# Kernel tuning notes

Hardware: AMD Instinct MI355X
Metric: run time of the kernel (lower is better)

Reference implementation:

```python
import jax, jax.numpy as jnp
import numpy as np

EPS = 1e-7  # tf.keras.backend.epsilon()


def squash(v, axis=-1):
    s = jnp.sum(jnp.square(v), axis=axis, keepdims=True)
    scale = s / (1.0 + s) / jnp.sqrt(s + EPS)
    return scale * v


def setup_inputs() -> dict:
    key = jax.random.key(0)
    k1, k2 = jax.random.split(key)
    B, I, D = 64, 2048, 16   # batch, input_num_capsule, input_dim_capsule
    J, K = 32, 16            # num_capsule, dim_capsule
    inputs = jax.random.normal(k1, (B, I, D), dtype=jnp.float32)
    # glorot_uniform-ish init for W: [in_caps, num_caps, in_dim, dim_caps]
    limit = np.sqrt(6.0 / (D + K)).astype(np.float32)
    W = jax.random.uniform(k2, (I, J, D, K), dtype=jnp.float32, minval=-limit, maxval=limit)
    return {"inputs": inputs, "W": W}


def reference(inputs, W, routings=3):
    # u_hat[b,i,j,:] = inputs[b,i,:] @ W[i,j,:,:]
    u_hat = jnp.einsum('bid,ijdk->bijk', inputs, W)  # [B, I, J, K]
    B, I, J, _ = u_hat.shape
    b = jnp.zeros((B, I, J, 1), dtype=u_hat.dtype)
    outputs = None
    for r in range(routings):
        c = jax.nn.softmax(b, axis=2)                              # [B, I, J, 1]
        outputs = squash(jnp.sum(c * u_hat, axis=1, keepdims=True))  # [B, 1, J, K]
        if r < routings - 1:
            b = b + jnp.sum(u_hat * outputs, axis=-1, keepdims=True)
    return jnp.squeeze(outputs, axis=1)  # [B, J, K]
```

## Files before the change

### kernel.cpp

```cpp
#include <hip/hip_runtime.h>
#include <hip/hip_bf16.h>


#define B_ 64
#define I_ 2048
#define D_ 16
#define J_ 32
#define K_ 16
#define JK 512
#define NBLK 256
#define GI 8

typedef __attribute__((ext_vector_type(8))) short short8;
typedef __attribute__((ext_vector_type(4))) float float4v;

__device__ __forceinline__ unsigned short f2bf(float f) {
    union { float f; unsigned int i; } v;
    v.f = f;
    const unsigned int x = v.i;
    return (unsigned short)((x + 0x7fffu + ((x >> 16) & 1u)) >> 16);
}

template <int MODE>
__global__ __launch_bounds__(512)
void caps_pass(const float* __restrict__ x, const float* __restrict__ W,
               const float* __restrict__ vsum, float* __restrict__ part) {
    __shared__ unsigned short wlds[2][32 * 384];
    __shared__ unsigned short zbuf[8];
    __shared__ float ebuf[2][4][2][16];
    const int tid = threadIdx.x;
    const int lane = tid & 63;
    const int wv = tid >> 6;
    const int bt = wv & 3;
    const int jh = wv >> 2;
    const int quad = lane >> 4;
    const int l15 = lane & 15;
    const int b = bt * 16 + l15;
    const int i0 = blockIdx.x * GI;

    if (tid < 8) zbuf[tid] = 0;

    float4 vv[16];
    if (MODE == 1) {
#pragma unroll
        for (int jj = 0; jj < 16; ++jj)
            vv[jj] = reinterpret_cast<const float4*>(
                vsum + b * JK + (jh * 16 + jj) * 16 + quad * 4)[0];
    }

    float4 acc2[16];
#pragma unroll
    for (int jj = 0; jj < 16; ++jj) {
        acc2[jj].x = 0.f; acc2[jj].y = 0.f;
        acc2[jj].z = 0.f; acc2[jj].w = 0.f;
    }

    const int sk = tid & 15;
    const int sj = tid >> 4;

    for (int t = 0; t < GI; ++t) {
        const int i = i0 + t;
        const int par = t & 1;

        {
            const float* p = W + (size_t)i * (J_ * D_ * K_) + sj * (D_ * K_) + sk;
            float vals[16];
#pragma unroll
            for (int d = 0; d < 16; ++d) vals[d] = p[d * K_];
            unsigned int pk[8];
#pragma unroll
            for (int q = 0; q < 8; ++q)
                pk[q] = ((unsigned int)f2bf(vals[2 * q + 1]) << 16) |
                        f2bf(vals[2 * q]);
            uint4* dst = reinterpret_cast<uint4*>(&wlds[par][sj * 384 + sk * 24]);
            uint4 w0; w0.x = pk[0]; w0.y = pk[1]; w0.z = pk[2]; w0.w = pk[3];
            uint4 w1; w1.x = pk[4]; w1.y = pk[5]; w1.z = pk[6]; w1.w = pk[7];
            dst[0] = w0; dst[1] = w1;
        }

        union { uint4 u; short8 s; } bfrag;
        {
            const float* xp = x + ((size_t)b * I_ + i) * D_ + (quad & 1) * 8;
            const float4 x0 = reinterpret_cast<const float4*>(xp)[0];
            const float4 x1 = reinterpret_cast<const float4*>(xp)[1];
            bfrag.u.x = ((unsigned int)f2bf(x0.y) << 16) | f2bf(x0.x);
            bfrag.u.y = ((unsigned int)f2bf(x0.w) << 16) | f2bf(x0.z);
            bfrag.u.z = ((unsigned int)f2bf(x1.y) << 16) | f2bf(x1.x);
            bfrag.u.w = ((unsigned int)f2bf(x1.w) << 16) | f2bf(x1.z);
            if (quad >= 2) { bfrag.u.x = 0; bfrag.u.y = 0; bfrag.u.z = 0; bfrag.u.w = 0; }
        }
        __syncthreads();

        const unsigned short* aptr =
            (quad >= 2) ? zbuf : (&wlds[par][0] + l15 * 24 + (quad & 1) * 8);
        const int astride = (quad >= 2) ? 0 : 384;

        if (MODE == 0) {
#pragma unroll
            for (int jj = 0; jj < 16; ++jj) {
                const int j = jh * 16 + jj;
                union { uint4 u; short8 s; } af;
                af.u = *reinterpret_cast<const uint4*>(aptr + (size_t)j * astride);
                float4v a = {0.f, 0.f, 0.f, 0.f};
                a = __builtin_amdgcn_mfma_f32_16x16x32_bf16(af.s, bfrag.s, a,
                                                            0, 0, 0);
                acc2[jj].x += a[0]; acc2[jj].y += a[1];
                acc2[jj].z += a[2]; acc2[jj].w += a[3];
            }
        } else {
            float e[16];
            float E = 0.f;
#pragma unroll
            for (int jj = 0; jj < 16; ++jj) {
                const int j = jh * 16 + jj;
                union { uint4 u; short8 s; } af;
                af.u = *reinterpret_cast<const uint4*>(aptr + (size_t)j * astride);
                float4v a = {0.f, 0.f, 0.f, 0.f};
                a = __builtin_amdgcn_mfma_f32_16x16x32_bf16(af.s, bfrag.s, a,
                                                            0, 0, 0);
                float p = a[0] * vv[jj].x + a[1] * vv[jj].y +
                          a[2] * vv[jj].z + a[3] * vv[jj].w;
                p += __shfl_xor(p, 16, 64);
                p += __shfl_xor(p, 32, 64);
                const float ee = __expf(p);
                e[jj] = ee;
                E += ee;
            }
            if (quad == 0) ebuf[par][bt][jh][l15] = E;
            __syncthreads();
            const float S = E + ebuf[par][bt][1 - jh][l15];
            const float r = __builtin_amdgcn_rcpf(S);
#pragma unroll
            for (int jj = 0; jj < 16; ++jj) {
                const int j = jh * 16 + jj;
                union { uint4 u; short8 s; } af;
                af.u = *reinterpret_cast<const uint4*>(aptr + (size_t)j * astride);
                float4v a = {0.f, 0.f, 0.f, 0.f};
                a = __builtin_amdgcn_mfma_f32_16x16x32_bf16(af.s, bfrag.s, a,
                                                            0, 0, 0);
                const float c = e[jj] * r;
                acc2[jj].x += c * a[0]; acc2[jj].y += c * a[1];
                acc2[jj].z += c * a[2]; acc2[jj].w += c * a[3];
            }
        }
    }

    float* pp = part + ((size_t)blockIdx.x * B_ + b) * JK + jh * 256 + quad * 4;
#pragma unroll
    for (int jj = 0; jj < 16; ++jj)
        reinterpret_cast<float4*>(pp + jj * 16)[0] = acc2[jj];
}

template <int MODE>
__global__ __launch_bounds__(512)
void caps_squashN(const float* __restrict__ part, float* __restrict__ vsum,
                  float* __restrict__ out) {
    const int bl = blockIdx.x;
    const int jk = threadIdx.x;
    float s = 0.f;
#pragma unroll 8
    for (int p = 0; p < NBLK; ++p)
        s += part[((size_t)p * B_ + bl) * JK + jk];
    if (MODE == 0) s *= (1.f / 32.f);
    float q = s * s;
    q += __shfl_xor(q, 1, 64);
    q += __shfl_xor(q, 2, 64);
    q += __shfl_xor(q, 4, 64);
    q += __shfl_xor(q, 8, 64);
    const float scale = q / ((1.f + q) * sqrtf(q + 1e-7f));
    const float v = scale * s;
    if (MODE == 0)      vsum[bl * JK + jk] = v;
    else if (MODE == 1) vsum[bl * JK + jk] += v;
    else                out[(size_t)bl * JK + jk] = v;
}

extern "C" void kernel_launch(void* const* d_in, const int* in_sizes, int n_in,
                              void* d_out, int out_size, void* d_ws,
                              size_t ws_size, hipStream_t stream) {
    const float* x = (const float*)d_in[0];
    const float* W = (const float*)d_in[1];
    float* out = (float*)d_out;

    char* ws = (char*)d_ws;
    float* part = (float*)ws;
    float* vsum =
        (float*)(ws + (size_t)B_ * I_ * JK * 2 + (size_t)64 * B_ * JK * 4);

    caps_pass<0><<<NBLK, 512, 0, stream>>>(x, W, nullptr, part);
    caps_squashN<0><<<B_, 512, 0, stream>>>(part, vsum, nullptr);
    caps_pass<1><<<NBLK, 512, 0, stream>>>(x, W, vsum, part);
    caps_squashN<1><<<B_, 512, 0, stream>>>(part, vsum, nullptr);
    caps_pass<1><<<NBLK, 512, 0, stream>>>(x, W, vsum, part);
    caps_squashN<2><<<B_, 512, 0, stream>>>(part, vsum, out);
}
```

Before: 229.9 us.

## Prefetch next W/x slice into registers and split squash reduction across more blocks

The caps_pass loop now loads the next capsule's W and x values into registers before the barrier and writes them to the alternate LDS buffer after compute. This overlaps global loads with MFMA work instead of stalling at the start of each iteration. The squash kernels launch four blocks per batch row, each covering 128 outputs, with four partial sums over the 256 block partials combined in shared memory. This adds parallelism to a reduction that was latency bound. The cost is higher register pressure from the prefetch buffers.

```diff
diff --git a/kernel.cpp b/kernel.cpp
--- a/kernel.cpp
+++ b/kernel.cpp
@@ -57,42 +57,51 @@
 
     const int sk = tid & 15;
     const int sj = tid >> 4;
+    const float* wp = W + (size_t)i0 * (J_ * D_ * K_) + sj * (D_ * K_) + sk;
+    const float* xp = x + ((size_t)b * I_ + i0) * D_ + (quad & 1) * 8;
+
+    float vals[16];
+#pragma unroll
+    for (int d = 0; d < 16; ++d) vals[d] = wp[d * K_];
+    float4 xr0 = reinterpret_cast<const float4*>(xp)[0];
+    float4 xr1 = reinterpret_cast<const float4*>(xp)[1];
+    {
+        unsigned int pk[8];
+#pragma unroll
+        for (int q = 0; q < 8; ++q)
+            pk[q] = ((unsigned int)f2bf(vals[2 * q + 1]) << 16) |
+                    f2bf(vals[2 * q]);
+        uint4* dst = reinterpret_cast<uint4*>(&wlds[0][sj * 384 + sk * 24]);
+        uint4 w0; w0.x = pk[0]; w0.y = pk[1]; w0.z = pk[2]; w0.w = pk[3];
+        uint4 w1; w1.x = pk[4]; w1.y = pk[5]; w1.z = pk[6]; w1.w = pk[7];
+        dst[0] = w0; dst[1] = w1;
+    }
 
     for (int t = 0; t < GI; ++t) {
-        const int i = i0 + t;
-        const int par = t & 1;
-
-        {
-            const float* p = W + (size_t)i * (J_ * D_ * K_) + sj * (D_ * K_) + sk;
-            float vals[16];
-#pragma unroll
-            for (int d = 0; d < 16; ++d) vals[d] = p[d * K_];
-            unsigned int pk[8];
-#pragma unroll
-            for (int q = 0; q < 8; ++q)
-                pk[q] = ((unsigned int)f2bf(vals[2 * q + 1]) << 16) |
-                        f2bf(vals[2 * q]);
-            uint4* dst = reinterpret_cast<uint4*>(&wlds[par][sj * 384 + sk * 24]);
-            uint4 w0; w0.x = pk[0]; w0.y = pk[1]; w0.z = pk[2]; w0.w = pk[3];
-            uint4 w1; w1.x = pk[4]; w1.y = pk[5]; w1.z = pk[6]; w1.w = pk[7];
-            dst[0] = w0; dst[1] = w1;
+        const int p = t & 1;
+
+        union { uint4 u; short8 s; } bfrag;
+        bfrag.u.x = ((unsigned int)f2bf(xr0.y) << 16) | f2bf(xr0.x);
+        bfrag.u.y = ((unsigned int)f2bf(xr0.w) << 16) | f2bf(xr0.z);
+        bfrag.u.z = ((unsigned int)f2bf(xr1.y) << 16) | f2bf(xr1.x);
+        bfrag.u.w = ((unsigned int)f2bf(xr1.w) << 16) | f2bf(xr1.z);
+        if (quad >= 2) { bfrag.u.x = 0; bfrag.u.y = 0; bfrag.u.z = 0; bfrag.u.w = 0; }
+
+        float nv[16];
+        float4 nx0, nx1;
+        if (t < GI - 1) {
+            const float* wn = wp + (size_t)(t + 1) * (J_ * D_ * K_);
+#pragma unroll
+            for (int d = 0; d < 16; ++d) nv[d] = wn[d * K_];
+            const float* xn = xp + (t + 1) * D_;
+            nx0 = reinterpret_cast<const float4*>(xn)[0];
+            nx1 = reinterpret_cast<const float4*>(xn)[1];
         }
 
-        union { uint4 u; short8 s; } bfrag;
-        {
-            const float* xp = x + ((size_t)b * I_ + i) * D_ + (quad & 1) * 8;
-            const float4 x0 = reinterpret_cast<const float4*>(xp)[0];
-            const float4 x1 = reinterpret_cast<const float4*>(xp)[1];
-            bfrag.u.x = ((unsigned int)f2bf(x0.y) << 16) | f2bf(x0.x);
-            bfrag.u.y = ((unsigned int)f2bf(x0.w) << 16) | f2bf(x0.z);
-            bfrag.u.z = ((unsigned int)f2bf(x1.y) << 16) | f2bf(x1.x);
-            bfrag.u.w = ((unsigned int)f2bf(x1.w) << 16) | f2bf(x1.z);
-            if (quad >= 2) { bfrag.u.x = 0; bfrag.u.y = 0; bfrag.u.z = 0; bfrag.u.w = 0; }
-        }
         __syncthreads();
 
         const unsigned short* aptr =
-            (quad >= 2) ? zbuf : (&wlds[par][0] + l15 * 24 + (quad & 1) * 8);
+            (quad >= 2) ? zbuf : (&wlds[p][0] + l15 * 24 + (quad & 1) * 8);
         const int astride = (quad >= 2) ? 0 : 384;
 
         if (MODE == 0) {
@@ -118,17 +127,17 @@
                 float4v a = {0.f, 0.f, 0.f, 0.f};
                 a = __builtin_amdgcn_mfma_f32_16x16x32_bf16(af.s, bfrag.s, a,
                                                             0, 0, 0);
-                float p = a[0] * vv[jj].x + a[1] * vv[jj].y +
-                          a[2] * vv[jj].z + a[3] * vv[jj].w;
-                p += __shfl_xor(p, 16, 64);
-                p += __shfl_xor(p, 32, 64);
-                const float ee = __expf(p);
+                float pj = a[0] * vv[jj].x + a[1] * vv[jj].y +
+                           a[2] * vv[jj].z + a[3] * vv[jj].w;
+                pj += __shfl_xor(pj, 16, 64);
+                pj += __shfl_xor(pj, 32, 64);
+                const float ee = __expf(pj);
                 e[jj] = ee;
                 E += ee;
             }
-            if (quad == 0) ebuf[par][bt][jh][l15] = E;
+            if (quad == 0) ebuf[p][bt][jh][l15] = E;
             __syncthreads();
-            const float S = E + ebuf[par][bt][1 - jh][l15];
+            const float S = E + ebuf[p][bt][1 - jh][l15];
             const float r = __builtin_amdgcn_rcpf(S);
 #pragma unroll
             for (int jj = 0; jj < 16; ++jj) {
@@ -143,6 +152,20 @@
                 acc2[jj].z += c * a[2]; acc2[jj].w += c * a[3];
             }
         }
+
+        if (t < GI - 1) {
+            unsigned int pk[8];
+#pragma unroll
+            for (int q = 0; q < 8; ++q)
+                pk[q] = ((unsigned int)f2bf(nv[2 * q + 1]) << 16) |
+                        f2bf(nv[2 * q]);
+            uint4* dst =
+                reinterpret_cast<uint4*>(&wlds[p ^ 1][sj * 384 + sk * 24]);
+            uint4 w0; w0.x = pk[0]; w0.y = pk[1]; w0.z = pk[2]; w0.w = pk[3];
+            uint4 w1; w1.x = pk[4]; w1.y = pk[5]; w1.z = pk[6]; w1.w = pk[7];
+            dst[0] = w0; dst[1] = w1;
+            xr0 = nx0; xr1 = nx1;
+        }
     }
 
     float* pp = part + ((size_t)blockIdx.x * B_ + b) * JK + jh * 256 + quad * 4;
@@ -155,23 +178,34 @@
 __global__ __launch_bounds__(512)
 void caps_squashN(const float* __restrict__ part, float* __restrict__ vsum,
                   float* __restrict__ out) {
-    const int bl = blockIdx.x;
-    const int jk = threadIdx.x;
+    __shared__ float red[3][128];
+    const int bl = blockIdx.x >> 2;
+    const int q4 = blockIdx.x & 3;
+    const int jk128 = threadIdx.x & 127;
+    const int h = threadIdx.x >> 7;
+    const int jk = q4 * 128 + jk128;
+
     float s = 0.f;
 #pragma unroll 8
-    for (int p = 0; p < NBLK; ++p)
+    for (int p = h * (NBLK / 4); p < (h + 1) * (NBLK / 4); ++p)
         s += part[((size_t)p * B_ + bl) * JK + jk];
-    if (MODE == 0) s *= (1.f / 32.f);
-    float q = s * s;
-    q += __shfl_xor(q, 1, 64);
-    q += __shfl_xor(q, 2, 64);
-    q += __shfl_xor(q, 4, 64);
-    q += __shfl_xor(q, 8, 64);
-    const float scale = q / ((1.f + q) * sqrtf(q + 1e-7f));
-    const float v = scale * s;
-    if (MODE == 0)      vsum[bl * JK + jk] = v;
-    else if (MODE == 1) vsum[bl * JK + jk] += v;
-    else                out[(size_t)bl * JK + jk] = v;
+
+    if (h > 0) red[h - 1][jk128] = s;
+    __syncthreads();
+    if (h == 0) {
+        s += red[0][jk128] + red[1][jk128] + red[2][jk128];
+        if (MODE == 0) s *= (1.f / 32.f);
+        float qq = s * s;
+        qq += __shfl_xor(qq, 1, 64);
+        qq += __shfl_xor(qq, 2, 64);
+        qq += __shfl_xor(qq, 4, 64);
+        qq += __shfl_xor(qq, 8, 64);
+        const float scale = qq / ((1.f + qq) * sqrtf(qq + 1e-7f));
+        const float v = scale * s;
+        if (MODE == 0)      vsum[bl * JK + jk] = v;
+        else if (MODE == 1) vsum[bl * JK + jk] += v;
+        else                out[(size_t)bl * JK + jk] = v;
+    }
 }
 
 extern "C" void kernel_launch(void* const* d_in, const int* in_sizes, int n_in,
@@ -187,9 +221,9 @@
         (float*)(ws + (size_t)B_ * I_ * JK * 2 + (size_t)64 * B_ * JK * 4);
 
     caps_pass<0><<<NBLK, 512, 0, stream>>>(x, W, nullptr, part);
-    caps_squashN<0><<<B_, 512, 0, stream>>>(part, vsum, nullptr);
+    caps_squashN<0><<<B_ * 4, 512, 0, stream>>>(part, vsum, nullptr);
     caps_pass<1><<<NBLK, 512, 0, stream>>>(x, W, vsum, part);
-    caps_squashN<1><<<B_, 512, 0, stream>>>(part, vsum, nullptr);
+    caps_squashN<1><<<B_ * 4, 512, 0, stream>>>(part, vsum, nullptr);
     caps_pass<1><<<NBLK, 512, 0, stream>>>(x, W, vsum, part);
-    caps_squashN<2><<<B_, 512, 0, stream>>>(part, vsum, out);
-}
+    caps_squashN<2><<<B_ * 4, 512, 0, stream>>>(part, vsum, out);
+}
```

New measurement: 191.5 us. -16.7%, faster.
